# Optimization experiments

Measured on AMD Instinct MI355X. Metric: run time of the kernel, lower is better.

Reference implementation:

```python
import jax, jax.numpy as jnp
import numpy as np

EPS_LN = 1e-5  # eqx.nn.LayerNorm default eps
DT_EPS = 1e-4  # softplus(dt) + 0.0001 in the module

H = 256  # hidden size
S = 256  # state size
B = 32
T = 4096


def setup_inputs() -> dict:
    key = jax.random.key(0)
    ks = jax.random.split(key, 8)
    sc = 1.0 / np.sqrt(H)
    return {
        "x": jax.random.normal(ks[0], (B, T, H), jnp.float32),
        "state0": jnp.zeros((B, S), jnp.float32),
        "in_to_state": jax.random.normal(ks[1], (S, H), jnp.float32) * sc,
        "state_to_hidden": jax.random.normal(ks[2], (H, S), jnp.float32) * sc,
        "direct": jax.random.normal(ks[3], (H,), jnp.float32) * sc,
        "a_diag": jax.random.normal(ks[4], (S,), jnp.float32),
        "g_diag": jax.random.normal(ks[5], (S,), jnp.float32),
        "dt": jax.random.normal(ks[6], (S,), jnp.float32) * 0.5 - 2.0,  # small timesteps
        "norm_w": jnp.ones((H,), jnp.float32),
        "norm_b": jnp.zeros((H,), jnp.float32),
        "out_w": jax.random.normal(ks[7], (H, H), jnp.float32) * sc,
        "out_b": jnp.zeros((H,), jnp.float32),
    }


def reference(x, state0, in_to_state, state_to_hidden, direct, a_diag, g_diag,
              dt, norm_w, norm_b, out_w, out_b):
    # Discretized diagonal oscillator coefficients (input-independent)
    dt_s = jax.nn.softplus(dt) + DT_EPS            # [S]
    omega = a_diag * dt_s                          # [S]
    decay = jnp.exp(-jax.nn.softplus(g_diag) * dt_s)
    decay = decay * decay                          # damped=True
    coeff = decay * jnp.cos(omega)                 # [S]

    # LayerNorm over feature dim (per-timestep, matching eqx.nn.LayerNorm)
    mu = jnp.mean(x, axis=-1, keepdims=True)
    var = jnp.var(x, axis=-1, keepdims=True)
    x_norm = (x - mu) * jax.lax.rsqrt(var + EPS_LN) * norm_w + norm_b  # [B,T,H]

    # Input injection: in_to_state @ x_norm for every timestep
    u = jnp.einsum("sh,bth->bts", in_to_state, x_norm)  # [B,T,S]

    # Diagonal linear recurrence: s_t = coeff * s_{t-1} + u_t
    def step(s, u_t):
        s = coeff * s + u_t
        return s, s

    u_t_major = jnp.swapaxes(u, 0, 1)                    # [T,B,S]
    final_state, states = jax.lax.scan(step, state0, u_t_major)
    states = jnp.swapaxes(states, 0, 1)                  # [B,T,S]

    # Readout + skip + gelu + out projection + residual
    mixed = jnp.einsum("hs,bts->bth", state_to_hidden, states) + direct * x_norm
    mixed = jax.nn.gelu(mixed)
    y = x + jnp.einsum("oh,bth->bto", out_w, mixed) + out_b
    return y, final_state
```

## Files before the change

### kernel.cpp

```cpp
#include <hip/hip_runtime.h>
#include <hip/hip_bf16.h>
#include <cstdint>
#include <cstddef>


typedef __bf16 bf16x8 __attribute__((ext_vector_type(8)));
typedef __bf16 bf16x4 __attribute__((ext_vector_type(4)));
typedef float  f32x4  __attribute__((ext_vector_type(4)));
typedef unsigned int u32x4 __attribute__((ext_vector_type(4)));

#define BB 32
#define TT 4096
#define HH 256
#define SS 256
#define MTOT (BB*TT)
#define NCHUNK 64
#define NT 8

__global__ void prep_kernel(const float* __restrict__ w1, const float* __restrict__ w2,
                            const float* __restrict__ w3,
                            __bf16* __restrict__ w1b, __bf16* __restrict__ w2b,
                            __bf16* __restrict__ w3b,
                            const float* __restrict__ a_diag, const float* __restrict__ g_diag,
                            const float* __restrict__ dt,
                            float* __restrict__ coeff, float* __restrict__ cL) {
    int i = blockIdx.x * 256 + threadIdx.x;
    w1b[i] = (__bf16)w1[i];
    w2b[i] = (__bf16)w2[i];
    w3b[i] = (__bf16)w3[i];
    if (i < SS) {
        float d = dt[i];
        float sp = (d > 20.f) ? d : log1pf(expf(d));
        float dts = sp + 1e-4f;
        float omega = a_diag[i] * dts;
        float gg = g_diag[i];
        float spg = (gg > 20.f) ? gg : log1pf(expf(gg));
        float dec = expf(-spg * dts);
        float c = dec * dec * cosf(omega);
        coeff[i] = c;
        float p = c;
        #pragma unroll
        for (int q = 0; q < 6; ++q) p = p * p;
        cL[i] = p;
    }
}

__global__ __launch_bounds__(256) void ln_kernel(const float* __restrict__ x,
                          const float* __restrict__ w, const float* __restrict__ b,
                          __bf16* __restrict__ xn) {
    int row = blockIdx.x * 4 + (threadIdx.x >> 6);
    int lane = threadIdx.x & 63;
    size_t base = (size_t)row * HH + lane * 4;
    const float4 v = *(const float4*)&x[base];
    float s  = v.x + v.y + v.z + v.w;
    float ss = v.x*v.x + v.y*v.y + v.z*v.z + v.w*v.w;
    #pragma unroll
    for (int off = 32; off; off >>= 1) {
        s  += __shfl_xor(s,  off, 64);
        ss += __shfl_xor(ss, off, 64);
    }
    float mu  = s * (1.f/256.f);
    float var = ss * (1.f/256.f) - mu*mu;
    float sc  = rsqrtf(var + 1e-5f);
    const float4 wv = *(const float4*)&w[lane*4];
    const float4 bv = *(const float4*)&b[lane*4];
    union { __bf16 h[4]; uint2 u; } pk;
    pk.h[0] = (__bf16)((v.x - mu)*sc*wv.x + bv.x);
    pk.h[1] = (__bf16)((v.y - mu)*sc*wv.y + bv.y);
    pk.h[2] = (__bf16)((v.z - mu)*sc*wv.z + bv.z);
    pk.h[3] = (__bf16)((v.w - mu)*sc*wv.w + bv.w);
    *(uint2*)&xn[base] = pk.u;
}

__device__ __forceinline__ void scan_xs_tile(__bf16* Xs, int tid, float c, float& st) {
    const int gb = tid >> 3, bo = (tid & 7) << 1;
    #pragma unroll
    for (int g4 = 0; g4 < 4; ++g4) {
        float v[8];
        #pragma unroll
        for (int r = 0; r < 8; ++r) {
            const int m = g4 * 8 + r;
            v[r] = (float)*(const __bf16*)((const char*)Xs + m * 512 + (((gb ^ (m & 15)) << 4) | bo));
        }
        __bf16 w[8];
        #pragma unroll
        for (int r = 0; r < 8; ++r) { st = c * st + v[r]; w[r] = (__bf16)st; }
        #pragma unroll
        for (int r = 0; r < 8; ++r) {
            const int m = g4 * 8 + r;
            *(__bf16*)((char*)Xs + m * 512 + (((gb ^ (m & 15)) << 4) | bo)) = w[r];
        }
    }
}

__device__ __forceinline__ void scan_es_carry(const __bf16* Es, int tid, float c, float& st) {
    const int gb = tid >> 2, bo = (tid & 3) << 1;
    #pragma unroll
    for (int g4 = 0; g4 < 4; ++g4) {
        float v[8];
        #pragma unroll
        for (int r = 0; r < 8; ++r) {
            const int m = g4 * 8 + r;
            v[r] = (float)*(const __bf16*)((const char*)Es + m * 512 + (((gb ^ ((m & 15) << 2)) << 3) | bo));
        }
        #pragma unroll
        for (int r = 0; r < 8; ++r) st = c * st + v[r];
    }
}

template<int MODE>
__global__ __launch_bounds__(512, 4) void gemm_kernel(
    const __bf16* __restrict__ W,
    const __bf16* __restrict__ X,
    void* Cout,
    const __bf16* xn_in,
    const float* __restrict__ dvec,
    const float* __restrict__ xres,
    const float* __restrict__ bias,
    const float* __restrict__ coeff,
    const float* __restrict__ state0,
    float* carry)
{
    __shared__ __bf16 Xs[32 * 256];
    __shared__ __bf16 Es[32 * 256];

    const int tid  = threadIdx.x;
    const int lane = tid & 63;
    const int wid  = tid >> 6;
    const int l15  = lane & 15, quad = lane >> 4;

    bf16x8 Wf[2][8];
    #pragma unroll
    for (int jn = 0; jn < 2; ++jn) {
        const int n = wid * 32 + jn * 16 + l15;
        #pragma unroll
        for (int kb = 0; kb < 8; ++kb)
            Wf[jn][kb] = *(const bf16x8*)&W[(size_t)n * 256 + kb * 32 + quad * 8];
    }

    const int bxi = blockIdx.x;
    const int bb  = bxi >> 4;
    const int chb = (bxi & 15) * 4;
    float c_s = 0.f, s0v = 0.f, cin0 = 0.f, cin1 = 0.f, cin2 = 0.f, cin3 = 0.f;
    if constexpr (MODE == 0) {
        if (tid < 256) {
            c_s = coeff[tid];
            if (chb == 0) s0v = state0[(size_t)bb * 256 + tid];
        }
    }
    if constexpr (MODE == 1) {
        if (tid < 256) {
            c_s = coeff[tid];
            cin0 = (chb == 0) ? state0[(size_t)bb * 256 + tid]
                              : carry[((size_t)bb * 64 + chb - 1) * 256 + tid];
            cin1 = carry[((size_t)bb * 64 + chb + 0) * 256 + tid];
            cin2 = carry[((size_t)bb * 64 + chb + 1) * 256 + tid];
            cin3 = carry[((size_t)bb * 64 + chb + 2) * 256 + tid];
        }
    }

    int sdst[2], srow[2];
    const int g = tid & 31;
    #pragma unroll
    for (int j = 0; j < 2; ++j) {
        const int m = j * 16 + (tid >> 5);
        srow[j] = m;
        sdst[j] = m * 512 + ((g ^ (m & 15)) * 16);
    }
    const int colb = g * 16;

    const size_t mbase = (size_t)bxi * 256;
    const char* Xb = (const char*)X;

    u32x4 pf[2];
    #pragma unroll
    for (int j = 0; j < 2; ++j)
        pf[j] = *(const u32x4*)(Xb + (mbase + srow[j]) * 512 + colb);
    #pragma unroll
    for (int j = 0; j < 2; ++j)
        *(u32x4*)((char*)Xs + sdst[j]) = pf[j];
    __syncthreads();
    #pragma unroll
    for (int j = 0; j < 2; ++j)
        pf[j] = *(const u32x4*)(Xb + (mbase + 32 + srow[j]) * 512 + colb);

    float st  = 0.f;
    float stc = 0.f;
    if constexpr (MODE == 1) {
        if (tid < 256) { st = cin0; scan_xs_tile(Xs, tid, c_s, st); }
        __syncthreads();
    }

    const int hrow = tid >> 5;
    const int nc   = tid & 31;

    for (int it = 0; it < NT; ++it) {
        const size_t mt0 = mbase + (size_t)it * 32;

        f32x4 acc[2][2] = {};
        #pragma unroll
        for (int kb = 0; kb < 8; ++kb) {
            bf16x8 xf[2];
            #pragma unroll
            for (int im = 0; im < 2; ++im)
                xf[im] = *(const bf16x8*)((const char*)Xs + (l15 + im * 16) * 512
                                          + (((kb * 4 + quad) ^ l15) * 16));
            #pragma unroll
            for (int jn = 0; jn < 2; ++jn)
                #pragma unroll
                for (int im = 0; im < 2; ++im)
                    acc[im][jn] = __builtin_amdgcn_mfma_f32_16x16x32_bf16(
                        Wf[jn][kb], xf[im], acc[im][jn], 0, 0, 0);
        }
        __syncthreads();

        if (it + 1 < NT) {
            #pragma unroll
            for (int j = 0; j < 2; ++j)
                *(u32x4*)((char*)Xs + sdst[j]) = pf[j];
        }
        #pragma unroll
        for (int im = 0; im < 2; ++im) {
            const int m = l15 + im * 16;
            #pragma unroll
            for (int jn = 0; jn < 2; ++jn) {
                const int gn = wid * 8 + jn * 4 + quad;
                bf16x4 pk;
                #pragma unroll
                for (int r = 0; r < 4; ++r) pk[r] = (__bf16)acc[im][jn][r];
                *(bf16x4*)((char*)Es + m * 512 + ((gn ^ (l15 << 2)) * 8)) = pk;
            }
        }
        __syncthreads();

        if (it + 2 < NT) {
            #pragma unroll
            for (int j = 0; j < 2; ++j)
                pf[j] = *(const u32x4*)(Xb + (mt0 + 64 + srow[j]) * 512 + colb);
        }

        if constexpr (MODE == 1) {
            if (it + 1 < NT && tid < 256) {
                const int itt = it + 1;
                if ((itt & 1) == 0) {
                    const int k = itt >> 1;
                    st = (k == 1) ? cin1 : (k == 2) ? cin2 : cin3;
                }
                scan_xs_tile(Xs, tid, c_s, st);
            }
        }

        #pragma unroll
        for (int r = 0; r < 2; ++r) {
            const int m = r * 16 + hrow;
            bf16x8 ev = *(const bf16x8*)((const char*)Es + m * 512 + (((nc * 2) ^ (hrow << 2)) * 8));
            const size_t gidx = (mt0 + m) * 256 + nc * 8;
            if (MODE == 0) {
                *(bf16x8*)((__bf16*)Cout + gidx) = ev;
            } else if (MODE == 1) {
                bf16x8 xv = *(const bf16x8*)&xn_in[gidx];
                f32x4 d0 = *(const f32x4*)&dvec[nc * 8];
                f32x4 d1 = *(const f32x4*)&dvec[nc * 8 + 4];
                bf16x8 pk;
                #pragma unroll
                for (int j = 0; j < 8; ++j) {
                    float dj = (j < 4) ? d0[j] : d1[j - 4];
                    float t = (float)ev[j] + dj * (float)xv[j];
                    float q = t + 0.044715f * t * t * t;
                    float e = __expf(-1.5957691216057308f * q);
                    pk[j] = (__bf16)(t * __builtin_amdgcn_rcpf(1.f + e));
                }
                *(bf16x8*)((__bf16*)Cout + gidx) = pk;
            } else {
                f32x4 x0 = *(const f32x4*)&xres[gidx];
                f32x4 x1 = *(const f32x4*)&xres[gidx + 4];
                f32x4 b0 = *(const f32x4*)&bias[nc * 8];
                f32x4 b1 = *(const f32x4*)&bias[nc * 8 + 4];
                f32x4 y0, y1;
                #pragma unroll
                for (int j = 0; j < 4; ++j) {
                    y0[j] = x0[j] + (float)ev[j]     + b0[j];
                    y1[j] = x1[j] + (float)ev[j + 4] + b1[j];
                }
                *(f32x4*)((float*)Cout + gidx)     = y0;
                *(f32x4*)((float*)Cout + gidx + 4) = y1;
            }
        }

        if constexpr (MODE == 0) {
            if (tid < 256) {
                if ((it & 1) == 0) stc = (it == 0 && chb == 0) ? s0v : 0.f;
                scan_es_carry(Es, tid, c_s, stc);
                if ((it & 1) == 1)
                    carry[((size_t)bb * 64 + (chb + (it >> 1))) * 256 + tid] = stc;
            }
        }

        if constexpr (MODE == 1) {
            if (it + 1 < NT) __syncthreads();
        }
    }
}

__global__ __launch_bounds__(256) void scan_prefix(float* carry, const float* __restrict__ cL,
                            float* __restrict__ fs_out) {
    int b = blockIdx.x, s = threadIdx.x;
    float cl = cL[s];
    float P = 0.f;
    for (int j = 0; j < NCHUNK; ++j) {
        int idx = (b * NCHUNK + j) * SS + s;
        P = cl * P + carry[idx];
        carry[idx] = P;
    }
    fs_out[b * SS + s] = P;
}

extern "C" void kernel_launch(void* const* d_in, const int* in_sizes, int n_in,
                              void* d_out, int out_size, void* d_ws, size_t ws_size,
                              hipStream_t stream) {
    const float* x      = (const float*)d_in[0];
    const float* state0 = (const float*)d_in[1];
    const float* w1     = (const float*)d_in[2];
    const float* w2     = (const float*)d_in[3];
    const float* direct = (const float*)d_in[4];
    const float* a_diag = (const float*)d_in[5];
    const float* g_diag = (const float*)d_in[6];
    const float* dt     = (const float*)d_in[7];
    const float* norm_w = (const float*)d_in[8];
    const float* norm_b = (const float*)d_in[9];
    const float* w3     = (const float*)d_in[10];
    const float* out_b  = (const float*)d_in[11];

    char* ws = (char*)d_ws;
    const size_t MH2 = (size_t)MTOT * HH * 2;
    __bf16* xn    = (__bf16*)(ws);
    __bf16* u     = (__bf16*)(ws + MH2);
    __bf16* w1b   = (__bf16*)(ws + 2*MH2);
    __bf16* w2b   = (__bf16*)(ws + 2*MH2 + 131072);
    __bf16* w3b   = (__bf16*)(ws + 2*MH2 + 262144);
    float*  coeff = (float*)(ws + 2*MH2 + 393216);
    float*  cL    = (float*)(ws + 2*MH2 + 394240);
    float*  carry = (float*)(ws + 2*MH2 + 395264);

    float* y_out  = (float*)d_out;
    float* fs_out = (float*)d_out + (size_t)MTOT * HH;

    prep_kernel<<<256, 256, 0, stream>>>(w1, w2, w3, w1b, w2b, w3b,
                                         a_diag, g_diag, dt, coeff, cL);
    ln_kernel<<<MTOT/4, 256, 0, stream>>>(x, norm_w, norm_b, xn);
    gemm_kernel<0><<<512, 512, 0, stream>>>(w1b, xn, u, nullptr, nullptr, nullptr, nullptr,
                                            coeff, state0, carry);
    scan_prefix<<<BB, 256, 0, stream>>>(carry, cL, fs_out);
    gemm_kernel<1><<<512, 512, 0, stream>>>(w2b, u, xn, xn, direct, nullptr, nullptr,
                                            coeff, state0, carry);
    gemm_kernel<2><<<512, 512, 0, stream>>>(w3b, xn, y_out, nullptr, nullptr, x, out_b,
                                            nullptr, nullptr, nullptr);
}
```

Measured before the change: 434.9 us.

## Fuse LayerNorm into first GEMM and merge readout with output projection

LayerNorm is computed inside the first GEMM kernel, which loads x in fp32, normalizes into the shared tile and also writes xn for later use. The second and third GEMMs are merged, so the GELU output stays in shared memory and feeds the out-projection directly, with W3 streamed from global memory. This removes one launch and the write and re-read of the intermediate mixed tensor. The scan_prefix loop is also batched to load eight carries at once. The cost is more shared memory, more barriers, and per-tile reloads of W3 in the fused kernel.

```diff
diff --git a/kernel.cpp b/kernel.cpp
--- a/kernel.cpp
+++ b/kernel.cpp
@@ -45,33 +45,6 @@
     }
 }
 
-__global__ __launch_bounds__(256) void ln_kernel(const float* __restrict__ x,
-                          const float* __restrict__ w, const float* __restrict__ b,
-                          __bf16* __restrict__ xn) {
-    int row = blockIdx.x * 4 + (threadIdx.x >> 6);
-    int lane = threadIdx.x & 63;
-    size_t base = (size_t)row * HH + lane * 4;
-    const float4 v = *(const float4*)&x[base];
-    float s  = v.x + v.y + v.z + v.w;
-    float ss = v.x*v.x + v.y*v.y + v.z*v.z + v.w*v.w;
-    #pragma unroll
-    for (int off = 32; off; off >>= 1) {
-        s  += __shfl_xor(s,  off, 64);
-        ss += __shfl_xor(ss, off, 64);
-    }
-    float mu  = s * (1.f/256.f);
-    float var = ss * (1.f/256.f) - mu*mu;
-    float sc  = rsqrtf(var + 1e-5f);
-    const float4 wv = *(const float4*)&w[lane*4];
-    const float4 bv = *(const float4*)&b[lane*4];
-    union { __bf16 h[4]; uint2 u; } pk;
-    pk.h[0] = (__bf16)((v.x - mu)*sc*wv.x + bv.x);
-    pk.h[1] = (__bf16)((v.y - mu)*sc*wv.y + bv.y);
-    pk.h[2] = (__bf16)((v.z - mu)*sc*wv.z + bv.z);
-    pk.h[3] = (__bf16)((v.w - mu)*sc*wv.w + bv.w);
-    *(uint2*)&xn[base] = pk.u;
-}
-
 __device__ __forceinline__ void scan_xs_tile(__bf16* Xs, int tid, float c, float& st) {
     const int gb = tid >> 3, bo = (tid & 7) << 1;
     #pragma unroll
@@ -108,18 +81,13 @@
     }
 }
 
-template<int MODE>
-__global__ __launch_bounds__(512, 4) void gemm_kernel(
+__global__ __launch_bounds__(512, 4) void gemm_ln_kernel(
     const __bf16* __restrict__ W,
-    const __bf16* __restrict__ X,
-    void* Cout,
-    const __bf16* xn_in,
-    const float* __restrict__ dvec,
-    const float* __restrict__ xres,
-    const float* __restrict__ bias,
-    const float* __restrict__ coeff,
-    const float* __restrict__ state0,
-    float* carry)
+    const float* __restrict__ x,
+    const float* __restrict__ nw, const float* __restrict__ nb,
+    __bf16* __restrict__ xn, __bf16* __restrict__ u,
+    const float* __restrict__ coeff, const float* __restrict__ state0,
+    float* __restrict__ carry)
 {
     __shared__ __bf16 Xs[32 * 256];
     __shared__ __bf16 Es[32 * 256];
@@ -141,22 +109,151 @@
     const int bxi = blockIdx.x;
     const int bb  = bxi >> 4;
     const int chb = (bxi & 15) * 4;
-    float c_s = 0.f, s0v = 0.f, cin0 = 0.f, cin1 = 0.f, cin2 = 0.f, cin3 = 0.f;
-    if constexpr (MODE == 0) {
+    float c_s = 0.f, s0v = 0.f;
+    if (tid < 256) {
+        c_s = coeff[tid];
+        if (chb == 0) s0v = state0[(size_t)bb * 256 + tid];
+    }
+
+    const f32x4 wn4 = *(const f32x4*)&nw[lane * 4];
+    const f32x4 bn4 = *(const f32x4*)&nb[lane * 4];
+
+    const size_t mbase = (size_t)bxi * 256;
+
+    f32x4 pf[4];
+    auto ln_load = [&](int tile) {
+        #pragma unroll
+        for (int j = 0; j < 4; ++j) {
+            const int m = j * 8 + wid;
+            pf[j] = *(const f32x4*)&x[(mbase + (size_t)tile * 32 + m) * 256 + lane * 4];
+        }
+    };
+    auto ln_store = [&](int tile) {
+        #pragma unroll
+        for (int j = 0; j < 4; ++j) {
+            const int m = j * 8 + wid;
+            f32x4 v = pf[j];
+            float s  = v[0] + v[1] + v[2] + v[3];
+            float ss = v[0]*v[0] + v[1]*v[1] + v[2]*v[2] + v[3]*v[3];
+            #pragma unroll
+            for (int off = 32; off; off >>= 1) {
+                s  += __shfl_xor(s,  off, 64);
+                ss += __shfl_xor(ss, off, 64);
+            }
+            float mu  = s * (1.f/256.f);
+            float var = ss * (1.f/256.f) - mu * mu;
+            float sc  = rsqrtf(var + 1e-5f);
+            bf16x4 pk;
+            #pragma unroll
+            for (int q2 = 0; q2 < 4; ++q2)
+                pk[q2] = (__bf16)((v[q2] - mu) * sc * wn4[q2] + bn4[q2]);
+            *(bf16x4*)((char*)Xs + m * 512 + ((((lane >> 1) ^ (m & 15)) << 4) | ((lane & 1) << 3))) = pk;
+            *(bf16x4*)&xn[(mbase + (size_t)tile * 32 + m) * 256 + lane * 4] = pk;
+        }
+    };
+
+    ln_load(0);
+    ln_store(0);
+    __syncthreads();
+    ln_load(1);
+
+    const int hrow = tid >> 5;
+    const int nc   = tid & 31;
+    float stc = 0.f;
+
+    for (int it = 0; it < NT; ++it) {
+        const size_t mt0 = mbase + (size_t)it * 32;
+
+        f32x4 acc[2][2] = {};
+        #pragma unroll
+        for (int kb = 0; kb < 8; ++kb) {
+            bf16x8 xf[2];
+            #pragma unroll
+            for (int im = 0; im < 2; ++im)
+                xf[im] = *(const bf16x8*)((const char*)Xs + (l15 + im * 16) * 512
+                                          + (((kb * 4 + quad) ^ l15) * 16));
+            #pragma unroll
+            for (int jn = 0; jn < 2; ++jn)
+                #pragma unroll
+                for (int im = 0; im < 2; ++im)
+                    acc[im][jn] = __builtin_amdgcn_mfma_f32_16x16x32_bf16(
+                        Wf[jn][kb], xf[im], acc[im][jn], 0, 0, 0);
+        }
+        __syncthreads();
+
+        if (it + 1 < NT) ln_store(it + 1);
+        #pragma unroll
+        for (int im = 0; im < 2; ++im) {
+            const int m = l15 + im * 16;
+            #pragma unroll
+            for (int jn = 0; jn < 2; ++jn) {
+                const int gn = wid * 8 + jn * 4 + quad;
+                bf16x4 pk;
+                #pragma unroll
+                for (int r = 0; r < 4; ++r) pk[r] = (__bf16)acc[im][jn][r];
+                *(bf16x4*)((char*)Es + m * 512 + ((gn ^ (l15 << 2)) * 8)) = pk;
+            }
+        }
+        __syncthreads();
+
+        if (it + 2 < NT) ln_load(it + 2);
+
+        #pragma unroll
+        for (int r = 0; r < 2; ++r) {
+            const int m = r * 16 + hrow;
+            bf16x8 ev = *(const bf16x8*)((const char*)Es + m * 512 + (((nc * 2) ^ (hrow << 2)) * 8));
+            *(bf16x8*)&u[(mt0 + m) * 256 + nc * 8] = ev;
+        }
+
         if (tid < 256) {
-            c_s = coeff[tid];
-            if (chb == 0) s0v = state0[(size_t)bb * 256 + tid];
-        }
-    }
-    if constexpr (MODE == 1) {
-        if (tid < 256) {
-            c_s = coeff[tid];
-            cin0 = (chb == 0) ? state0[(size_t)bb * 256 + tid]
-                              : carry[((size_t)bb * 64 + chb - 1) * 256 + tid];
-            cin1 = carry[((size_t)bb * 64 + chb + 0) * 256 + tid];
-            cin2 = carry[((size_t)bb * 64 + chb + 1) * 256 + tid];
-            cin3 = carry[((size_t)bb * 64 + chb + 2) * 256 + tid];
-        }
+            if ((it & 1) == 0) stc = (it == 0 && chb == 0) ? s0v : 0.f;
+            scan_es_carry(Es, tid, c_s, stc);
+            if ((it & 1) == 1)
+                carry[((size_t)bb * 64 + (chb + (it >> 1))) * 256 + tid] = stc;
+        }
+    }
+}
+
+__global__ __launch_bounds__(512, 4) void gemm_fused_kernel(
+    const __bf16* __restrict__ W2, const __bf16* __restrict__ W3,
+    const __bf16* __restrict__ u, const __bf16* __restrict__ xn,
+    const float* __restrict__ dvec,
+    const float* __restrict__ xres, const float* __restrict__ bias,
+    const float* __restrict__ coeff, const float* __restrict__ state0,
+    const float* __restrict__ carry,
+    float* __restrict__ y)
+{
+    __shared__ __bf16 Xs [32 * 256];
+    __shared__ __bf16 Es [32 * 256];
+    __shared__ __bf16 Xs2[32 * 256];
+
+    const int tid  = threadIdx.x;
+    const int lane = tid & 63;
+    const int wid  = tid >> 6;
+    const int l15  = lane & 15, quad = lane >> 4;
+
+    bf16x8 W2f[2][8];
+    #pragma unroll
+    for (int jn = 0; jn < 2; ++jn) {
+        const int n = wid * 32 + jn * 16 + l15;
+        #pragma unroll
+        for (int kb = 0; kb < 8; ++kb)
+            W2f[jn][kb] = *(const bf16x8*)&W2[(size_t)n * 256 + kb * 32 + quad * 8];
+    }
+    const __bf16* w3p0 = W3 + (size_t)(wid * 32 + l15) * 256 + quad * 8;
+    const __bf16* w3p1 = w3p0 + 16 * 256;
+
+    const int bxi = blockIdx.x;
+    const int bb  = bxi >> 4;
+    const int chb = (bxi & 15) * 4;
+    float c_s = 0.f, cin0 = 0.f, cin1 = 0.f, cin2 = 0.f, cin3 = 0.f;
+    if (tid < 256) {
+        c_s  = coeff[tid];
+        cin0 = (chb == 0) ? state0[(size_t)bb * 256 + tid]
+                          : carry[((size_t)bb * 64 + chb - 1) * 256 + tid];
+        cin1 = carry[((size_t)bb * 64 + chb + 0) * 256 + tid];
+        cin2 = carry[((size_t)bb * 64 + chb + 1) * 256 + tid];
+        cin3 = carry[((size_t)bb * 64 + chb + 2) * 256 + tid];
     }
 
     int sdst[2], srow[2];
@@ -168,28 +265,24 @@
         sdst[j] = m * 512 + ((g ^ (m & 15)) * 16);
     }
     const int colb = g * 16;
-
     const size_t mbase = (size_t)bxi * 256;
-    const char* Xb = (const char*)X;
+    const char* Ub = (const char*)u;
 
     u32x4 pf[2];
     #pragma unroll
     for (int j = 0; j < 2; ++j)
-        pf[j] = *(const u32x4*)(Xb + (mbase + srow[j]) * 512 + colb);
+        pf[j] = *(const u32x4*)(Ub + (mbase + srow[j]) * 512 + colb);
     #pragma unroll
     for (int j = 0; j < 2; ++j)
         *(u32x4*)((char*)Xs + sdst[j]) = pf[j];
     __syncthreads();
     #pragma unroll
     for (int j = 0; j < 2; ++j)
-        pf[j] = *(const u32x4*)(Xb + (mbase + 32 + srow[j]) * 512 + colb);
-
-    float st  = 0.f;
-    float stc = 0.f;
-    if constexpr (MODE == 1) {
-        if (tid < 256) { st = cin0; scan_xs_tile(Xs, tid, c_s, st); }
-        __syncthreads();
-    }
+        pf[j] = *(const u32x4*)(Ub + (mbase + 32 + srow[j]) * 512 + colb);
+
+    float st = 0.f;
+    if (tid < 256) { st = cin0; scan_xs_tile(Xs, tid, c_s, st); }
+    __syncthreads();
 
     const int hrow = tid >> 5;
     const int nc   = tid & 31;
@@ -210,7 +303,7 @@
                 #pragma unroll
                 for (int im = 0; im < 2; ++im)
                     acc[im][jn] = __builtin_amdgcn_mfma_f32_16x16x32_bf16(
-                        Wf[jn][kb], xf[im], acc[im][jn], 0, 0, 0);
+                        W2f[jn][kb], xf[im], acc[im][jn], 0, 0, 0);
         }
         __syncthreads();
 
@@ -236,18 +329,15 @@
         if (it + 2 < NT) {
             #pragma unroll
             for (int j = 0; j < 2; ++j)
-                pf[j] = *(const u32x4*)(Xb + (mt0 + 64 + srow[j]) * 512 + colb);
-        }
-
-        if constexpr (MODE == 1) {
-            if (it + 1 < NT && tid < 256) {
-                const int itt = it + 1;
-                if ((itt & 1) == 0) {
-                    const int k = itt >> 1;
-                    st = (k == 1) ? cin1 : (k == 2) ? cin2 : cin3;
-                }
-                scan_xs_tile(Xs, tid, c_s, st);
-            }
+                pf[j] = *(const u32x4*)(Ub + (mt0 + 64 + srow[j]) * 512 + colb);
+        }
+        if (it + 1 < NT && tid < 256) {
+            const int itt = it + 1;
+            if ((itt & 1) == 0) {
+                const int k = itt >> 1;
+                st = (k == 1) ? cin1 : (k == 2) ? cin2 : cin3;
+            }
+            scan_xs_tile(Xs, tid, c_s, st);
         }
 
         #pragma unroll
@@ -255,49 +345,79 @@
             const int m = r * 16 + hrow;
             bf16x8 ev = *(const bf16x8*)((const char*)Es + m * 512 + (((nc * 2) ^ (hrow << 2)) * 8));
             const size_t gidx = (mt0 + m) * 256 + nc * 8;
-            if (MODE == 0) {
-                *(bf16x8*)((__bf16*)Cout + gidx) = ev;
-            } else if (MODE == 1) {
-                bf16x8 xv = *(const bf16x8*)&xn_in[gidx];
-                f32x4 d0 = *(const f32x4*)&dvec[nc * 8];
-                f32x4 d1 = *(const f32x4*)&dvec[nc * 8 + 4];
-                bf16x8 pk;
-                #pragma unroll
-                for (int j = 0; j < 8; ++j) {
-                    float dj = (j < 4) ? d0[j] : d1[j - 4];
-                    float t = (float)ev[j] + dj * (float)xv[j];
-                    float q = t + 0.044715f * t * t * t;
-                    float e = __expf(-1.5957691216057308f * q);
-                    pk[j] = (__bf16)(t * __builtin_amdgcn_rcpf(1.f + e));
-                }
-                *(bf16x8*)((__bf16*)Cout + gidx) = pk;
-            } else {
-                f32x4 x0 = *(const f32x4*)&xres[gidx];
-                f32x4 x1 = *(const f32x4*)&xres[gidx + 4];
-                f32x4 b0 = *(const f32x4*)&bias[nc * 8];
-                f32x4 b1 = *(const f32x4*)&bias[nc * 8 + 4];
-                f32x4 y0, y1;
-                #pragma unroll
-                for (int j = 0; j < 4; ++j) {
-                    y0[j] = x0[j] + (float)ev[j]     + b0[j];
-                    y1[j] = x1[j] + (float)ev[j + 4] + b1[j];
-                }
-                *(f32x4*)((float*)Cout + gidx)     = y0;
-                *(f32x4*)((float*)Cout + gidx + 4) = y1;
-            }
-        }
-
-        if constexpr (MODE == 0) {
-            if (tid < 256) {
-                if ((it & 1) == 0) stc = (it == 0 && chb == 0) ? s0v : 0.f;
-                scan_es_carry(Es, tid, c_s, stc);
-                if ((it & 1) == 1)
-                    carry[((size_t)bb * 64 + (chb + (it >> 1))) * 256 + tid] = stc;
-            }
-        }
-
-        if constexpr (MODE == 1) {
-            if (it + 1 < NT) __syncthreads();
+            bf16x8 xv = *(const bf16x8*)&xn[gidx];
+            f32x4 d0 = *(const f32x4*)&dvec[nc * 8];
+            f32x4 d1 = *(const f32x4*)&dvec[nc * 8 + 4];
+            bf16x8 pk;
+            #pragma unroll
+            for (int jj = 0; jj < 8; ++jj) {
+                float dj = (jj < 4) ? d0[jj] : d1[jj - 4];
+                float t = (float)ev[jj] + dj * (float)xv[jj];
+                float q = t + 0.044715f * t * t * t;
+                float e = __expf(-1.5957691216057308f * q);
+                pk[jj] = (__bf16)(t * __builtin_amdgcn_rcpf(1.f + e));
+            }
+            *(bf16x8*)((char*)Xs2 + m * 512 + ((nc ^ (m & 15)) * 16)) = pk;
+        }
+        __syncthreads();
+
+        f32x4 acc2[2][2] = {};
+        bf16x8 wr[3][2];
+        wr[0][0] = *(const bf16x8*)(w3p0);
+        wr[0][1] = *(const bf16x8*)(w3p1);
+        wr[1][0] = *(const bf16x8*)(w3p0 + 32);
+        wr[1][1] = *(const bf16x8*)(w3p1 + 32);
+        #pragma unroll
+        for (int kb = 0; kb < 8; ++kb) {
+            if (kb + 2 < 8) {
+                wr[(kb + 2) % 3][0] = *(const bf16x8*)(w3p0 + (kb + 2) * 32);
+                wr[(kb + 2) % 3][1] = *(const bf16x8*)(w3p1 + (kb + 2) * 32);
+            }
+            bf16x8 xf[2];
+            #pragma unroll
+            for (int im = 0; im < 2; ++im)
+                xf[im] = *(const bf16x8*)((const char*)Xs2 + (l15 + im * 16) * 512
+                                          + (((kb * 4 + quad) ^ l15) * 16));
+            #pragma unroll
+            for (int jn = 0; jn < 2; ++jn)
+                #pragma unroll
+                for (int im = 0; im < 2; ++im)
+                    acc2[im][jn] = __builtin_amdgcn_mfma_f32_16x16x32_bf16(
+                        wr[kb % 3][jn], xf[im], acc2[im][jn], 0, 0, 0);
+        }
+        __syncthreads();
+
+        #pragma unroll
+        for (int im = 0; im < 2; ++im) {
+            const int m = l15 + im * 16;
+            #pragma unroll
+            for (int jn = 0; jn < 2; ++jn) {
+                const int gn = wid * 8 + jn * 4 + quad;
+                bf16x4 pk;
+                #pragma unroll
+                for (int r = 0; r < 4; ++r) pk[r] = (__bf16)acc2[im][jn][r];
+                *(bf16x4*)((char*)Es + m * 512 + ((gn ^ (l15 << 2)) * 8)) = pk;
+            }
+        }
+        __syncthreads();
+
+        #pragma unroll
+        for (int r = 0; r < 2; ++r) {
+            const int m = r * 16 + hrow;
+            bf16x8 ev = *(const bf16x8*)((const char*)Es + m * 512 + (((nc * 2) ^ (hrow << 2)) * 8));
+            const size_t gidx = (mt0 + m) * 256 + nc * 8;
+            f32x4 x0 = *(const f32x4*)&xres[gidx];
+            f32x4 x1 = *(const f32x4*)&xres[gidx + 4];
+            f32x4 b0 = *(const f32x4*)&bias[nc * 8];
+            f32x4 b1 = *(const f32x4*)&bias[nc * 8 + 4];
+            f32x4 y0, y1;
+            #pragma unroll
+            for (int jj = 0; jj < 4; ++jj) {
+                y0[jj] = x0[jj] + (float)ev[jj]     + b0[jj];
+                y1[jj] = x1[jj] + (float)ev[jj + 4] + b1[jj];
+            }
+            *(f32x4*)&y[gidx]     = y0;
+            *(f32x4*)&y[gidx + 4] = y1;
         }
     }
 }
@@ -307,10 +427,18 @@
     int b = blockIdx.x, s = threadIdx.x;
     float cl = cL[s];
     float P = 0.f;
-    for (int j = 0; j < NCHUNK; ++j) {
-        int idx = (b * NCHUNK + j) * SS + s;
-        P = cl * P + carry[idx];
-        carry[idx] = P;
+    #pragma unroll
+    for (int jo = 0; jo < 8; ++jo) {
+        float v[8];
+        #pragma unroll
+        for (int r = 0; r < 8; ++r)
+            v[r] = carry[((size_t)b * NCHUNK + jo * 8 + r) * SS + s];
+        float w[8];
+        #pragma unroll
+        for (int r = 0; r < 8; ++r) { P = cl * P + v[r]; w[r] = P; }
+        #pragma unroll
+        for (int r = 0; r < 8; ++r)
+            carry[((size_t)b * NCHUNK + jo * 8 + r) * SS + s] = w[r];
     }
     fs_out[b * SS + s] = P;
 }
@@ -347,12 +475,9 @@
 
     prep_kernel<<<256, 256, 0, stream>>>(w1, w2, w3, w1b, w2b, w3b,
                                          a_diag, g_diag, dt, coeff, cL);
-    ln_kernel<<<MTOT/4, 256, 0, stream>>>(x, norm_w, norm_b, xn);
-    gemm_kernel<0><<<512, 512, 0, stream>>>(w1b, xn, u, nullptr, nullptr, nullptr, nullptr,
+    gemm_ln_kernel<<<512, 512, 0, stream>>>(w1b, x, norm_w, norm_b, xn, u,
                                             coeff, state0, carry);
     scan_prefix<<<BB, 256, 0, stream>>>(carry, cL, fs_out);
-    gemm_kernel<1><<<512, 512, 0, stream>>>(w2b, u, xn, xn, direct, nullptr, nullptr,
-                                            coeff, state0, carry);
-    gemm_kernel<2><<<512, 512, 0, stream>>>(w3b, xn, y_out, nullptr, nullptr, x, out_b,
-                                            nullptr, nullptr, nullptr);
-}
+    gemm_fused_kernel<<<512, 512, 0, stream>>>(w2b, w3b, u, xn, direct, x, out_b,
+                                               coeff, state0, carry, y_out);
+}
```

New measurement: 552.5 us. 1.27x slower.
